# Performance work log

Measured on AMD Instinct MI355X. Metric: run time of the kernel, lower is better.

The kernel has to match this reference:

```python
import jax, jax.numpy as jnp
import numpy as np

C = 64
CK = C // 8  # query/key channels

def setup_inputs() -> dict:
    key = jax.random.key(0)
    ks = jax.random.split(key, 8)
    x = jax.random.normal(ks[0], (4, C, 16, 16, 16), dtype=jnp.float32)
    # 1x1x1 Conv3d weights collapse to [out_ch, in_ch] matrices
    wq = jax.random.normal(ks[1], (CK, C), dtype=jnp.float32) * (1.0 / np.sqrt(C))
    bq = jax.random.normal(ks[2], (CK,), dtype=jnp.float32) * 0.01
    wk = jax.random.normal(ks[3], (CK, C), dtype=jnp.float32) * (1.0 / np.sqrt(C))
    bk = jax.random.normal(ks[4], (CK,), dtype=jnp.float32) * 0.01
    wv = jax.random.normal(ks[5], (C, C), dtype=jnp.float32) * (1.0 / np.sqrt(C))
    bv = jax.random.normal(ks[6], (C,), dtype=jnp.float32) * 0.01
    gamma = jnp.ones((1,), dtype=jnp.float32) * 0.5  # nonzero so attention path affects output
    return {"x": x, "wq": wq, "bq": bq, "wk": wk, "bk": bk, "wv": wv, "bv": bv, "gamma": gamma}

def reference(x, wq, bq, wk, bk, wv, bv, gamma):
    B, Cc, D, H, W = x.shape
    N = D * H * W
    xf = x.reshape(B, Cc, N)  # [B, C, N]
    q = jnp.einsum('kc,bcn->bkn', wq, xf) + bq[None, :, None]  # [B, CK, N]
    k = jnp.einsum('kc,bcn->bkn', wk, xf) + bk[None, :, None]  # [B, CK, N]
    v = jnp.einsum('oc,bcn->bon', wv, xf) + bv[None, :, None]  # [B, C, N]
    # energy[b,i,j] = sum_k q[b,k,i] * k[b,k,j]; softmax over j (no scaling, per source)
    energy = jnp.einsum('bki,bkj->bij', q, k)  # [B, N, N]
    attn = jax.nn.softmax(energy, axis=-1)
    # out[b,c,i] = sum_j v[b,c,j] * attn[b,i,j]
    out = jnp.einsum('bcj,bij->bci', v, attn)  # [B, C, N]
    out = out.reshape(B, Cc, D, H, W)
    return gamma * out + x
```

## Files before the change

### kernel.cpp

```cpp
#include <hip/hip_runtime.h>
#include <hip/hip_bf16.h>

#define BATCH  4
#define CDIM   64
#define CKD    8
#define NPOS   4096
#define RLN2   1.44269504f
#define SH2    25.96851039f
#define ECL2   14.42695041f
#define PTP    72

typedef _Float16 f16x8 __attribute__((ext_vector_type(8)));
typedef float    f32x4 __attribute__((ext_vector_type(4)));

__device__ __forceinline__ f16x8 pack8(const float* e) {
    f16x8 v;
#pragma unroll
    for (int i = 0; i < 8; ++i) v[i] = (_Float16)e[i];
    return v;
}

__device__ __forceinline__ void gl_lds16(const void* g, void* l) {
    __builtin_amdgcn_global_load_lds(
        (const __attribute__((address_space(1))) void*)g,
        (__attribute__((address_space(3))) void*)l, 16, 0, 0);
}
__device__ __forceinline__ void gl_lds4(const void* g, void* l) {
    __builtin_amdgcn_global_load_lds(
        (const __attribute__((address_space(1))) void*)g,
        (__attribute__((address_space(3))) void*)l, 4, 0, 0);
}

__global__ __launch_bounds__(256, 4) void proj_kernel(
    const float* __restrict__ x,
    const float* __restrict__ wq, const float* __restrict__ bq,
    const float* __restrict__ wk, const float* __restrict__ bk,
    const float* __restrict__ wv, const float* __restrict__ bv,
    _Float16* __restrict__ qh, _Float16* __restrict__ kh,
    _Float16* __restrict__ vswz)
{
    __shared__ float red[64 * 73];

    const int bid  = blockIdx.x;
    const int part = bid >> 8;
    const int tid  = threadIdx.x;
    const int s    = tid & 63;
    const int h    = tid >> 6;
    const int pos  = (bid & 255) * 64 + s;
    const int b    = pos >> 12;
    const int n    = pos & 4095;
    const int c0   = part * 16;
    const int cl0  = h * 16;

    const float* xb = x + (size_t)b * CDIM * NPOS + n;

    float vacc[16];
#pragma unroll
    for (int o = 0; o < 16; ++o) vacc[o] = 0.f;
    float qacc[8] = {0.f, 0.f, 0.f, 0.f, 0.f, 0.f, 0.f, 0.f};

    if (part < 2) {
        const float* wqk = (part == 0) ? wq : wk;
#pragma unroll
        for (int cc = 0; cc < 16; ++cc) {
            const int c = cl0 + cc;
            const float xv = xb[(size_t)c * NPOS];
#pragma unroll
            for (int o = 0; o < 8; ++o)  qacc[o] = fmaf(wqk[o * CDIM + c], xv, qacc[o]);
#pragma unroll
            for (int o = 0; o < 16; ++o) vacc[o] = fmaf(wv[(c0 + o) * CDIM + c], xv, vacc[o]);
        }
    } else {
#pragma unroll
        for (int cc = 0; cc < 16; ++cc) {
            const int c = cl0 + cc;
            const float xv = xb[(size_t)c * NPOS];
#pragma unroll
            for (int o = 0; o < 16; ++o) vacc[o] = fmaf(wv[(c0 + o) * CDIM + c], xv, vacc[o]);
        }
    }

    float* rs = red + s * 73;
    if (h != 0) {
        float* rh = rs + (h - 1) * 24;
        if (part < 2) {
#pragma unroll
            for (int i = 0; i < 8; ++i)  rh[i] = qacc[i];
#pragma unroll
            for (int o = 0; o < 16; ++o) rh[8 + o] = vacc[o];
        } else {
#pragma unroll
            for (int o = 0; o < 16; ++o) rh[o] = vacc[o];
        }
    }
    __syncthreads();
    if (h != 0) return;

    if (part < 2) {
#pragma unroll
        for (int i = 0; i < 8; ++i)  qacc[i] += rs[i] + rs[24 + i] + rs[48 + i];
#pragma unroll
        for (int o = 0; o < 16; ++o) vacc[o] += rs[8 + o] + rs[32 + o] + rs[56 + o];

        const float* bqk = (part == 0) ? bq : bk;
        const float scl  = (part == 0) ? RLN2 : 1.0f;
        f16x8 qv;
#pragma unroll
        for (int o = 0; o < 8; ++o) qv[o] = (_Float16)((qacc[o] + bqk[o]) * scl);
        _Float16* dst = ((part == 0) ? qh : kh) + ((size_t)(b * NPOS + n)) * CKD;
        *(f16x8*)dst = qv;
    } else {
#pragma unroll
        for (int o = 0; o < 16; ++o) vacc[o] += rs[o] + rs[24 + o] + rs[48 + o];
    }

    const int jq = (n >> 2) & 3;
    const int ju = ((n >> 4) & 1) * 4 + (n & 3);
    const size_t vbase = (size_t)(b * 128 + (n >> 5)) * 2048 + jq * 8 + ju;
#pragma unroll
    for (int o = 0; o < 16; ++o)
        vswz[vbase + (size_t)(c0 + o) * 32] = (_Float16)(vacc[o] + bv[c0 + o]);
}

template<int NSPLIT>
__global__ __launch_bounds__(256, 4) void attn_kernel(
    const _Float16* __restrict__ qh, const _Float16* __restrict__ kh,
    const _Float16* __restrict__ vswz,
    __hip_bfloat16* __restrict__ po, float* __restrict__ pl)
{
    constexpr int JCHUNK = NPOS / NSPLIT;
    constexpr int NIT32  = JCHUNK / 32;

    __shared__ __align__(16) _Float16 vbuf[2][2048];
    __shared__ __align__(16) _Float16 kbuf[2][256];
    __shared__ __hip_bfloat16 pt[4][16][PTP];

    const int bid   = blockIdx.x;
    const int split = bid & (NSPLIT - 1);
    const int itile = (bid / NSPLIT) & 31;
    const int b     = bid / (NSPLIT * 32);
    const int tid   = threadIdx.x;
    const int wave  = tid >> 6;
    const int lane  = tid & 63;
    const int quad  = lane >> 4;
    const int m16   = lane & 15;

    const int i0 = itile * 128 + wave * 32;

    f16x8 qa0 = *(const f16x8*)(qh + ((size_t)(b * NPOS + i0 + m16)) * CKD);
    f16x8 qa1 = *(const f16x8*)(qh + ((size_t)(b * NPOS + i0 + 16 + m16)) * CKD);
    if (quad != 0) { qa0 = (f16x8){}; qa1 = (f16x8){}; }

    const _Float16* vsrc = vswz + (size_t)b * 262144
                         + (size_t)split * (JCHUNK / 32) * 2048
                         + wave * 512 + lane * 8;
    const _Float16* ksrc = kh + ((size_t)(b * NPOS + split * JCHUNK)) * CKD
                         + wave * 128 + lane * 2;

    f32x4 acc0[4], acc1[4];
#pragma unroll
    for (int nb = 0; nb < 4; ++nb) {
        acc0[nb] = (f32x4){0.f, 0.f, 0.f, 0.f};
        acc1[nb] = (f32x4){0.f, 0.f, 0.f, 0.f};
    }
    float ls0 = 0.f, ls1 = 0.f;
    const f32x4 csh = {-SH2, -SH2, -SH2, -SH2};

    gl_lds16(vsrc, &vbuf[0][wave * 512]);
    if (wave < 2) gl_lds4(ksrc, &kbuf[0][wave * 128]);
    asm volatile("s_waitcnt vmcnt(0)" ::: "memory");
    __builtin_amdgcn_s_barrier();

    int cur = 0;
    for (int it = 0; it < NIT32; ++it) {
        gl_lds16(vsrc + (size_t)(it + 1) * 2048, &vbuf[cur ^ 1][wave * 512]);
        if (wave < 2) gl_lds4(ksrc + (size_t)(it + 1) * 256, &kbuf[cur ^ 1][wave * 128]);

        const f16x8 kfa = *(const f16x8*)(&kbuf[cur][m16 * 8]);
        const f16x8 kfb = *(const f16x8*)(&kbuf[cur][128 + m16 * 8]);

        __builtin_amdgcn_s_setprio(1);
        const f32x4 s0a = __builtin_amdgcn_mfma_f32_16x16x32_f16(kfa, qa0, csh, 0, 0, 0);
        const f32x4 s0b = __builtin_amdgcn_mfma_f32_16x16x32_f16(kfb, qa0, csh, 0, 0, 0);
        const f32x4 s1a = __builtin_amdgcn_mfma_f32_16x16x32_f16(kfa, qa1, csh, 0, 0, 0);
        const f32x4 s1b = __builtin_amdgcn_mfma_f32_16x16x32_f16(kfb, qa1, csh, 0, 0, 0);
        __builtin_amdgcn_s_setprio(0);

        float e0[8], e1[8];
#pragma unroll
        for (int r = 0; r < 4; ++r) {
            e0[r]     = __builtin_exp2f(fminf(s0a[r], ECL2));
            e0[4 + r] = __builtin_exp2f(fminf(s0b[r], ECL2));
            e1[r]     = __builtin_exp2f(fminf(s1a[r], ECL2));
            e1[4 + r] = __builtin_exp2f(fminf(s1b[r], ECL2));
        }
        ls0 += ((e0[0] + e0[1]) + (e0[2] + e0[3])) + ((e0[4] + e0[5]) + (e0[6] + e0[7]));
        ls1 += ((e1[0] + e1[1]) + (e1[2] + e1[3])) + ((e1[4] + e1[5]) + (e1[6] + e1[7]));

        const f16x8 pa0 = pack8(e0);
        const f16x8 pa1 = pack8(e1);

        __builtin_amdgcn_s_setprio(1);
#pragma unroll
        for (int nb = 0; nb < 4; ++nb) {
            const f16x8 vb = *(const f16x8*)(&vbuf[cur][m16 * 32 + quad * 8 + nb * 512]);
            acc0[nb] = __builtin_amdgcn_mfma_f32_16x16x32_f16(pa0, vb, acc0[nb], 0, 0, 0);
            acc1[nb] = __builtin_amdgcn_mfma_f32_16x16x32_f16(pa1, vb, acc1[nb], 0, 0, 0);
        }
        __builtin_amdgcn_s_setprio(0);

        asm volatile("s_waitcnt vmcnt(0)" ::: "memory");
        __builtin_amdgcn_s_barrier();
        cur ^= 1;
    }

    ls0 += __shfl_xor(ls0, 16);
    ls0 += __shfl_xor(ls0, 32);
    ls1 += __shfl_xor(ls1, 16);
    ls1 += __shfl_xor(ls1, 32);

    const int sbx = split * BATCH + b;
    if (quad == 0) {
        pl[(size_t)sbx * NPOS + i0 + m16]      = ls0;
        pl[(size_t)sbx * NPOS + i0 + 16 + m16] = ls1;
    }

    __hip_bfloat16* ept = &pt[wave][0][0];

#define EPILOG(ACC, IOFS)                                                     \
    do {                                                                      \
        _Pragma("unroll")                                                     \
        for (int nb = 0; nb < 4; ++nb)                                        \
            _Pragma("unroll")                                                 \
            for (int r = 0; r < 4; ++r)                                       \
                ept[(quad * 4 + r) * PTP + nb * 16 + m16] =                   \
                    __float2bfloat16(ACC[nb][r]);                             \
        _Pragma("unroll")                                                     \
        for (int g2 = 0; g2 < 16; ++g2) {                                     \
            const int c = quad + g2 * 4;                                      \
            po[((size_t)sbx * CDIM + c) * NPOS + i0 + (IOFS) + m16] =         \
                ept[m16 * PTP + c];                                           \
        }                                                                     \
    } while (0)

    EPILOG(acc0, 0);
    EPILOG(acc1, 16);
#undef EPILOG
}

template<int NSPLIT>
__global__ __launch_bounds__(256) void combine_kernel(
    const float* __restrict__ x,
    const __hip_bfloat16* __restrict__ po, const float* __restrict__ pl,
    const float* __restrict__ gamma, float* __restrict__ out)
{
    const int t  = blockIdx.x * 256 + threadIdx.x;
    const int i4 = (t & 1023) * 4;
    const int c  = (t >> 10) & 63;
    const int b  = t >> 16;

    const unsigned short* pou = (const unsigned short*)po;

    float L0 = 0.f, L1 = 0.f, L2 = 0.f, L3 = 0.f;
    float O0 = 0.f, O1 = 0.f, O2 = 0.f, O3 = 0.f;
#pragma unroll
    for (int s = 0; s < NSPLIT; ++s) {
        const size_t sb = (size_t)(s * BATCH + b);
        const float4 lv = *(const float4*)(pl + sb * NPOS + i4);
        const ushort4 pv = *(const ushort4*)(pou + (sb * CDIM + c) * NPOS + i4);
        L0 += lv.x; L1 += lv.y; L2 += lv.z; L3 += lv.w;
        O0 += __uint_as_float((unsigned)pv.x << 16);
        O1 += __uint_as_float((unsigned)pv.y << 16);
        O2 += __uint_as_float((unsigned)pv.z << 16);
        O3 += __uint_as_float((unsigned)pv.w << 16);
    }
    const float g = gamma[0];
    const size_t xi = ((size_t)(b * CDIM + c)) * NPOS + i4;
    const float4 xv = *(const float4*)(x + xi);
    float4 o;
    o.x = fmaf(g, O0 / L0, xv.x);
    o.y = fmaf(g, O1 / L1, xv.y);
    o.z = fmaf(g, O2 / L2, xv.z);
    o.w = fmaf(g, O3 / L3, xv.w);
    *(float4*)(out + xi) = o;
}

extern "C" void kernel_launch(void* const* d_in, const int* in_sizes, int n_in,
                              void* d_out, int out_size, void* d_ws, size_t ws_size,
                              hipStream_t stream)
{
    const float* x     = (const float*)d_in[0];
    const float* wq    = (const float*)d_in[1];
    const float* bq    = (const float*)d_in[2];
    const float* wk    = (const float*)d_in[3];
    const float* bk    = (const float*)d_in[4];
    const float* wv    = (const float*)d_in[5];
    const float* bv    = (const float*)d_in[6];
    const float* gamma = (const float*)d_in[7];
    float* out = (float*)d_out;

    char* ws = (char*)d_ws;
    _Float16*       qh   = (_Float16*)(ws);
    _Float16*       kh   = (_Float16*)(ws + (256 << 10));
    _Float16*       vswz = (_Float16*)(ws + (512 << 10));
    __hip_bfloat16* po   = (__hip_bfloat16*)(ws + (2560 << 10));

    const size_t po8_end = (2560ull << 10) + 8ull * 4 * CDIM * NPOS * 2;
    const size_t need8   = po8_end + 8ull * 4 * NPOS * 4;

    proj_kernel<<<1024, 256, 0, stream>>>(x, wq, bq, wk, bk, wv, bv, qh, kh, vswz);

    if (ws_size >= need8) {
        float* pl = (float*)(ws + po8_end);
        attn_kernel<8><<<BATCH * 32 * 8, 256, 0, stream>>>(qh, kh, vswz, po, pl);
        combine_kernel<8><<<1024, 256, 0, stream>>>(x, po, pl, gamma, out);
    } else {
        const size_t po4_end = (2560ull << 10) + 4ull * 4 * CDIM * NPOS * 2;
        float* pl = (float*)(ws + po4_end);
        attn_kernel<4><<<BATCH * 32 * 4, 256, 0, stream>>>(qh, kh, vswz, po, pl);
        combine_kernel<4><<<1024, 256, 0, stream>>>(x, po, pl, gamma, out);
    }
}
```

Measured before the change: 122.2 us.

## Double attention j-tile per barrier and load K fragments directly from global

The attention loop now processes 64 key positions per iteration instead of 32, staging twice as much V into LDS per double-buffer slot so half as many barriers and waitcnts are needed. The K tile is no longer staged through LDS; each lane reads its K fragment straight from global memory, which is likely cached. This cuts synchronization and LDS traffic, but doubles the LDS buffer size and exposes K global-load latency inside the compute loop, which may hurt occupancy or stall the MFMAs.

```diff
diff --git a/kernel.cpp b/kernel.cpp
--- a/kernel.cpp
+++ b/kernel.cpp
@@ -24,11 +24,6 @@
     __builtin_amdgcn_global_load_lds(
         (const __attribute__((address_space(1))) void*)g,
         (__attribute__((address_space(3))) void*)l, 16, 0, 0);
-}
-__device__ __forceinline__ void gl_lds4(const void* g, void* l) {
-    __builtin_amdgcn_global_load_lds(
-        (const __attribute__((address_space(1))) void*)g,
-        (__attribute__((address_space(3))) void*)l, 4, 0, 0);
 }
 
 __global__ __launch_bounds__(256, 4) void proj_kernel(
@@ -129,10 +124,9 @@
     __hip_bfloat16* __restrict__ po, float* __restrict__ pl)
 {
     constexpr int JCHUNK = NPOS / NSPLIT;
-    constexpr int NIT32  = JCHUNK / 32;
-
-    __shared__ __align__(16) _Float16 vbuf[2][2048];
-    __shared__ __align__(16) _Float16 kbuf[2][256];
+    constexpr int NIT64  = JCHUNK / 64;
+
+    __shared__ __align__(16) _Float16 vbuf[2][4096];
     __shared__ __hip_bfloat16 pt[4][16][PTP];
 
     const int bid   = blockIdx.x;
@@ -151,11 +145,11 @@
     f16x8 qa1 = *(const f16x8*)(qh + ((size_t)(b * NPOS + i0 + 16 + m16)) * CKD);
     if (quad != 0) { qa0 = (f16x8){}; qa1 = (f16x8){}; }
 
+    const _Float16* kp = kh + ((size_t)(b * NPOS + split * JCHUNK) + (size_t)m16) * CKD;
+
     const _Float16* vsrc = vswz + (size_t)b * 262144
                          + (size_t)split * (JCHUNK / 32) * 2048
-                         + wave * 512 + lane * 8;
-    const _Float16* ksrc = kh + ((size_t)(b * NPOS + split * JCHUNK)) * CKD
-                         + wave * 128 + lane * 2;
+                         + wave * 1024 + lane * 8;
 
     f32x4 acc0[4], acc1[4];
 #pragma unroll
@@ -166,48 +160,55 @@
     float ls0 = 0.f, ls1 = 0.f;
     const f32x4 csh = {-SH2, -SH2, -SH2, -SH2};
 
-    gl_lds16(vsrc, &vbuf[0][wave * 512]);
-    if (wave < 2) gl_lds4(ksrc, &kbuf[0][wave * 128]);
+    gl_lds16(vsrc,       &vbuf[0][wave * 1024]);
+    gl_lds16(vsrc + 512, &vbuf[0][wave * 1024 + 512]);
     asm volatile("s_waitcnt vmcnt(0)" ::: "memory");
     __builtin_amdgcn_s_barrier();
 
     int cur = 0;
-    for (int it = 0; it < NIT32; ++it) {
-        gl_lds16(vsrc + (size_t)(it + 1) * 2048, &vbuf[cur ^ 1][wave * 512]);
-        if (wave < 2) gl_lds4(ksrc + (size_t)(it + 1) * 256, &kbuf[cur ^ 1][wave * 128]);
-
-        const f16x8 kfa = *(const f16x8*)(&kbuf[cur][m16 * 8]);
-        const f16x8 kfb = *(const f16x8*)(&kbuf[cur][128 + m16 * 8]);
-
-        __builtin_amdgcn_s_setprio(1);
-        const f32x4 s0a = __builtin_amdgcn_mfma_f32_16x16x32_f16(kfa, qa0, csh, 0, 0, 0);
-        const f32x4 s0b = __builtin_amdgcn_mfma_f32_16x16x32_f16(kfb, qa0, csh, 0, 0, 0);
-        const f32x4 s1a = __builtin_amdgcn_mfma_f32_16x16x32_f16(kfa, qa1, csh, 0, 0, 0);
-        const f32x4 s1b = __builtin_amdgcn_mfma_f32_16x16x32_f16(kfb, qa1, csh, 0, 0, 0);
-        __builtin_amdgcn_s_setprio(0);
-
-        float e0[8], e1[8];
-#pragma unroll
-        for (int r = 0; r < 4; ++r) {
-            e0[r]     = __builtin_exp2f(fminf(s0a[r], ECL2));
-            e0[4 + r] = __builtin_exp2f(fminf(s0b[r], ECL2));
-            e1[r]     = __builtin_exp2f(fminf(s1a[r], ECL2));
-            e1[4 + r] = __builtin_exp2f(fminf(s1b[r], ECL2));
-        }
-        ls0 += ((e0[0] + e0[1]) + (e0[2] + e0[3])) + ((e0[4] + e0[5]) + (e0[6] + e0[7]));
-        ls1 += ((e1[0] + e1[1]) + (e1[2] + e1[3])) + ((e1[4] + e1[5]) + (e1[6] + e1[7]));
-
-        const f16x8 pa0 = pack8(e0);
-        const f16x8 pa1 = pack8(e1);
-
-        __builtin_amdgcn_s_setprio(1);
-#pragma unroll
-        for (int nb = 0; nb < 4; ++nb) {
-            const f16x8 vb = *(const f16x8*)(&vbuf[cur][m16 * 32 + quad * 8 + nb * 512]);
-            acc0[nb] = __builtin_amdgcn_mfma_f32_16x16x32_f16(pa0, vb, acc0[nb], 0, 0, 0);
-            acc1[nb] = __builtin_amdgcn_mfma_f32_16x16x32_f16(pa1, vb, acc1[nb], 0, 0, 0);
-        }
-        __builtin_amdgcn_s_setprio(0);
+    for (int it = 0; it < NIT64; ++it) {
+        {
+            const _Float16* vn = vsrc + (size_t)(it + 1) * 4096;
+            gl_lds16(vn,       &vbuf[cur ^ 1][wave * 1024]);
+            gl_lds16(vn + 512, &vbuf[cur ^ 1][wave * 1024 + 512]);
+        }
+
+#pragma unroll
+        for (int h = 0; h < 2; ++h) {
+            const f16x8 kfa = *(const f16x8*)(kp + (size_t)(h * 32) * CKD);
+            const f16x8 kfb = *(const f16x8*)(kp + (size_t)(h * 32 + 16) * CKD);
+
+            __builtin_amdgcn_s_setprio(1);
+            const f32x4 s0a = __builtin_amdgcn_mfma_f32_16x16x32_f16(kfa, qa0, csh, 0, 0, 0);
+            const f32x4 s0b = __builtin_amdgcn_mfma_f32_16x16x32_f16(kfb, qa0, csh, 0, 0, 0);
+            const f32x4 s1a = __builtin_amdgcn_mfma_f32_16x16x32_f16(kfa, qa1, csh, 0, 0, 0);
+            const f32x4 s1b = __builtin_amdgcn_mfma_f32_16x16x32_f16(kfb, qa1, csh, 0, 0, 0);
+            __builtin_amdgcn_s_setprio(0);
+
+            float e0[8], e1[8];
+#pragma unroll
+            for (int r = 0; r < 4; ++r) {
+                e0[r]     = __builtin_exp2f(fminf(s0a[r], ECL2));
+                e0[4 + r] = __builtin_exp2f(fminf(s0b[r], ECL2));
+                e1[r]     = __builtin_exp2f(fminf(s1a[r], ECL2));
+                e1[4 + r] = __builtin_exp2f(fminf(s1b[r], ECL2));
+            }
+            ls0 += ((e0[0] + e0[1]) + (e0[2] + e0[3])) + ((e0[4] + e0[5]) + (e0[6] + e0[7]));
+            ls1 += ((e1[0] + e1[1]) + (e1[2] + e1[3])) + ((e1[4] + e1[5]) + (e1[6] + e1[7]));
+
+            const f16x8 pa0 = pack8(e0);
+            const f16x8 pa1 = pack8(e1);
+
+            __builtin_amdgcn_s_setprio(1);
+#pragma unroll
+            for (int nb = 0; nb < 4; ++nb) {
+                const f16x8 vb = *(const f16x8*)(&vbuf[cur][h * 2048 + m16 * 32 + quad * 8 + nb * 512]);
+                acc0[nb] = __builtin_amdgcn_mfma_f32_16x16x32_f16(pa0, vb, acc0[nb], 0, 0, 0);
+                acc1[nb] = __builtin_amdgcn_mfma_f32_16x16x32_f16(pa1, vb, acc1[nb], 0, 0, 0);
+            }
+            __builtin_amdgcn_s_setprio(0);
+        }
+        kp += 64 * CKD;
 
         asm volatile("s_waitcnt vmcnt(0)" ::: "memory");
         __builtin_amdgcn_s_barrier();
```

Result: no change. 122.6 us (+0.3%).
